# Kernel optimization log

Hardware: AMD Instinct MI355X
Metric: run time of the kernel (lower is better)

Reference implementation:

```python
import jax, jax.numpy as jnp
import numpy as np

BATCH = 16
MAX_SEQLEN = 8192
D_MODEL = 1024
TOTAL = 65536  # sum of sequence lengths


def setup_inputs() -> dict:
    key = jax.random.key(0)
    k_buf, _ = jax.random.split(key)
    # Position buffer (e.g. precomputed position embeddings), first dim >= max length.
    buffer = jax.random.normal(k_buf, (MAX_SEQLEN, D_MODEL), dtype=jnp.float32)
    # Build ragged offsets: BATCH lengths, each <= MAX_SEQLEN, summing to TOTAL.
    rng = np.random.default_rng(0)
    base = TOTAL // BATCH  # 4096
    d = rng.integers(0, 2048, size=BATCH // 2)
    lengths = np.concatenate([base + d, base - d])
    rng.shuffle(lengths)
    offsets = jnp.asarray(np.concatenate([[0], np.cumsum(lengths)]), dtype=jnp.int32)
    return {"buffer": buffer, "offsets": offsets, "total_tokens": TOTAL}


def reference(buffer, offsets, total_tokens):
    # Equivalent of: for each sequence i with length L_i = offsets[i+1]-offsets[i],
    # take buffer[:L_i]; concatenate into jagged values sharing the same offsets.
    # Done in one vectorized pass: local position of each flat token = idx - offsets[seg].
    idx = jnp.arange(total_tokens, dtype=jnp.int32)                      # [T]
    seg = jnp.searchsorted(offsets, idx, side="right") - 1              # [T] sequence id
    pos = idx - offsets[seg]                                             # [T] ragged arange
    values = buffer[pos]                                                 # [T, D] jagged values
    return values
```

## Files before the change

### kernel.cpp

```cpp
#include <hip/hip_runtime.h>


#define D_MODEL 1024
#define VEC4_PER_ROW (D_MODEL / 4)
#define MAX_OFFSETS 64

__global__ __launch_bounds__(256) void positionid_gather(
    const float4* __restrict__ buf,
    const int*    __restrict__ offsets,
    int n_off,
    float4*       __restrict__ out)
{
    const int t = blockIdx.x;

    int seg = 0;
    #pragma unroll 4
    for (int i = 1; i < n_off - 1; ++i) {
        if (offsets[i] <= t) seg = i;
    }
    const int pos = t - offsets[seg];

    out[(size_t)t * VEC4_PER_ROW + threadIdx.x] =
        buf[(size_t)pos * VEC4_PER_ROW + threadIdx.x];
}

extern "C" void kernel_launch(void* const* d_in, const int* in_sizes, int n_in,
                              void* d_out, int out_size, void* d_ws, size_t ws_size,
                              hipStream_t stream) {
    const float4* buf     = (const float4*)d_in[0];
    const int*    offsets = (const int*)d_in[1];
    const int     n_off   = in_sizes[1];
    float4*       out     = (float4*)d_out;

    const int T = out_size / D_MODEL;

    positionid_gather<<<dim3(T), dim3(256), 0, stream>>>(buf, offsets, n_off, out);
}
```

Before: 306.0 us.

## Process multiple rows per block with batched loads and nontemporal stores

Each block now handles 32 output rows instead of one. The offsets are staged once in shared memory and the segment index is advanced incrementally rather than searched in full for every row. Loads are issued in groups of 8 before the stores to keep more memory requests in flight, and the output is written with nontemporal stores to avoid polluting the cache. The trade-off is fewer blocks and higher register pressure per thread.

New measurement: 309.9 us. No clear change (+1.3%).

```diff
diff --git a/kernel.cpp b/kernel.cpp
--- a/kernel.cpp
+++ b/kernel.cpp
@@ -2,37 +2,72 @@
 
 
 #define D_MODEL 1024
-#define VEC4_PER_ROW (D_MODEL / 4)
-#define MAX_OFFSETS 64
+#define V4 (D_MODEL / 4)
+#define ROWS_PER_BLOCK 32
+#define UNROLL 8
+#define MAX_OFF 64
 
-__global__ __launch_bounds__(256) void positionid_gather(
-    const float4* __restrict__ buf,
-    const int*    __restrict__ offsets,
+typedef float v4f __attribute__((ext_vector_type(4)));
+
+__global__ __launch_bounds__(256, 8) void positionid_gather(
+    const v4f* __restrict__ buf,
+    const int* __restrict__ offsets,
     int n_off,
-    float4*       __restrict__ out)
+    v4f*       __restrict__ out,
+    int T)
 {
-    const int t = blockIdx.x;
+    __shared__ int soff[MAX_OFF];
+    const int tid = threadIdx.x;
+    if (tid < n_off) soff[tid] = offsets[tid];
+    __syncthreads();
+
+    const int t0 = blockIdx.x * ROWS_PER_BLOCK;
+    if (t0 >= T) return;
 
     int seg = 0;
-    #pragma unroll 4
-    for (int i = 1; i < n_off - 1; ++i) {
-        if (offsets[i] <= t) seg = i;
+    while (seg + 2 < n_off && soff[seg + 1] <= t0) ++seg;
+
+    if (t0 + ROWS_PER_BLOCK <= T) {
+        for (int r = 0; r < ROWS_PER_BLOCK; r += UNROLL) {
+            int pos[UNROLL];
+            #pragma unroll
+            for (int k = 0; k < UNROLL; ++k) {
+                const int t = t0 + r + k;
+                while (seg + 2 < n_off && soff[seg + 1] <= t) ++seg;
+                pos[k] = t - soff[seg];
+            }
+            v4f v[UNROLL];
+            #pragma unroll
+            for (int k = 0; k < UNROLL; ++k)
+                v[k] = buf[(size_t)pos[k] * V4 + tid];
+            #pragma unroll
+            for (int k = 0; k < UNROLL; ++k)
+                __builtin_nontemporal_store(
+                    v[k], &out[(size_t)(t0 + r + k) * V4 + tid]);
+        }
+    } else {
+        for (int r = 0; r < ROWS_PER_BLOCK; ++r) {
+            const int t = t0 + r;
+            if (t >= T) break;
+            while (seg + 2 < n_off && soff[seg + 1] <= t) ++seg;
+            const int pos = t - soff[seg];
+            v4f v = buf[(size_t)pos * V4 + tid];
+            __builtin_nontemporal_store(v, &out[(size_t)t * V4 + tid]);
+        }
     }
-    const int pos = t - offsets[seg];
-
-    out[(size_t)t * VEC4_PER_ROW + threadIdx.x] =
-        buf[(size_t)pos * VEC4_PER_ROW + threadIdx.x];
 }
 
 extern "C" void kernel_launch(void* const* d_in, const int* in_sizes, int n_in,
                               void* d_out, int out_size, void* d_ws, size_t ws_size,
                               hipStream_t stream) {
-    const float4* buf     = (const float4*)d_in[0];
-    const int*    offsets = (const int*)d_in[1];
-    const int     n_off   = in_sizes[1];
-    float4*       out     = (float4*)d_out;
+    const v4f* buf     = (const v4f*)d_in[0];
+    const int* offsets = (const int*)d_in[1];
+    const int  n_off   = in_sizes[1];
+    v4f*       out     = (v4f*)d_out;
 
     const int T = out_size / D_MODEL;
 
-    positionid_gather<<<dim3(T), dim3(256), 0, stream>>>(buf, offsets, n_off, out);
+    const int nblocks = (T + ROWS_PER_BLOCK - 1) / ROWS_PER_BLOCK;
+    positionid_gather<<<dim3(nblocks), dim3(256), 0, stream>>>(
+        buf, offsets, n_off, out, T);
 }
```
